# Kernel optimization log

Measured on AMD Instinct MI355X. Metric: run time of the kernel, lower is better.

Reference implementation:

```python
import jax, jax.numpy as jnp
import numpy as np

# Search geometry (matches init_kwargs)
WS, WT, PS, K, STRIDE0 = 9, 1, 7, 10, 4
SEARCH_INPUT = "noisy"
ALPHA = 0.5
CRIT = "l2"


def _extract_patches(vid, ti, hi, wi):
    """vid: [T,H,W,C]; ti/hi/wi int32 with shape [...] (patch top-left corners).
    Returns [..., PS*PS*C] with clamped (edge-replicated) boundary handling."""
    T, H, W, C = vid.shape
    dy = jnp.arange(PS)
    dx = jnp.arange(PS)
    hh = jnp.clip(hi[..., None, None] + dy[:, None], 0, H - 1)  # [...,PS,1]
    ww = jnp.clip(wi[..., None, None] + dx[None, :], 0, W - 1)  # [...,1,PS]
    p = vid[ti[..., None, None], hh, ww]  # [...,PS,PS,C]
    return p.reshape(p.shape[:-3] + (PS * PS * C,))


def _nls(vid, fflow, bflow):
    """NonLocalSearch: vid [T,H,W,C], flows [T,H,W,2] (channel 0 = x/w, 1 = y/h).
    Returns (topk_dists [nq,K], inds = (ti,hi,wi,tk,hk,wk))."""
    T, H, W, C = vid.shape
    nH, nW = H // STRIDE0, W // STRIDE0
    ti, hi, wi = jnp.meshgrid(jnp.arange(T), jnp.arange(nH) * STRIDE0,
                              jnp.arange(nW) * STRIDE0, indexing="ij")
    ti, hi, wi = ti.reshape(-1), hi.reshape(-1), wi.reshape(-1)  # [nq]
    q = _extract_patches(vid, ti, hi, wi)  # [nq, PS*PS*C]

    ff = fflow[ti, hi, wi]  # [nq,2] flow to frame t+1
    bf = bflow[ti, hi, wi]  # [nq,2] flow to frame t-1
    zero = jnp.zeros_like(ff)
    flow_dt = jnp.stack([bf, zero, ff], axis=1)  # [nq, 2*WT+1, 2] for dt=-1,0,+1
    dts = jnp.arange(-WT, WT + 1)
    tj = jnp.clip(ti[:, None] + dts[None, :], 0, T - 1)  # [nq, 2*WT+1]
    bh = jnp.clip(hi[:, None] + jnp.round(flow_dt[..., 1]).astype(jnp.int32), 0, H - 1)
    bw = jnp.clip(wi[:, None] + jnp.round(flow_dt[..., 0]).astype(jnp.int32), 0, W - 1)

    # Candidate schedule: (dt_index, oy, ox) for all (2*WT+1)*WS*WS candidates.
    r = WS // 2
    oy, ox = np.meshgrid(np.arange(-r, r + 1), np.arange(-r, r + 1), indexing="ij")
    nt = 2 * WT + 1
    specs = np.stack([np.repeat(np.arange(nt), WS * WS),
                      np.tile(oy.ravel(), nt),
                      np.tile(ox.ravel(), nt)], axis=1).astype(np.int32)  # [S,3]

    def step(_, spec):
        di, sy, sx = spec[0], spec[1], spec[2]
        tjc = tj[:, di]
        hj = jnp.clip(bh[:, di] + sy, 0, H - 1)
        wj = jnp.clip(bw[:, di] + sx, 0, W - 1)
        cp = _extract_patches(vid, tjc, hj, wj)  # [nq,D]
        d = jnp.sum((q - cp) ** 2, axis=-1)  # L2 patch distance, [nq]
        return None, (d, tjc, hj, wj)

    _, (dists, tjs, hjs, wjs) = jax.lax.scan(step, None, jnp.asarray(specs))
    # dists: [S, nq] -> top-K smallest per query
    negd, idx = jax.lax.top_k(-dists.T, K)  # [nq,K]
    tk = jnp.take_along_axis(tjs.T, idx, axis=1)
    hk = jnp.take_along_axis(hjs.T, idx, axis=1)
    wk = jnp.take_along_axis(wjs.T, idx, axis=1)
    return -negd, (ti, hi, wi, tk, hk, wk)


def _refine(vid, inds):
    """RefineSearch with wr=1,kr=1: recompute L2 patch distances at given inds."""
    ti, hi, wi, tk, hk, wk = inds
    q = _extract_patches(vid, ti, hi, wi)          # [nq, D]
    cp = _extract_patches(vid, tk, hk, wk)         # [nq, K, D]
    return jnp.sum((q[:, None, :] - cp) ** 2, axis=-1)  # [nq, K]


def setup_inputs() -> dict:
    key = jax.random.key(0)
    k1, k2, k3, k4 = jax.random.split(key, 4)
    B, T, C, H, W = 1, 5, 3, 384, 384
    noisy = jax.random.normal(k1, (B, T, C, H, W), dtype=jnp.float32)
    deno = jax.random.normal(k2, (B, T, C, H, W), dtype=jnp.float32)
    fflow = jax.random.normal(k3, (B, T, 2, H, W), dtype=jnp.float32)
    bflow = jax.random.normal(k4, (B, T, 2, H, W), dtype=jnp.float32)
    return {"noisy": noisy, "deno": deno, "fflow": fflow, "bflow": bflow}


def reference(noisy, deno, fflow, bflow):
    def per_video(nv, dv, ff, bf):
        nv_t = jnp.transpose(nv, (0, 2, 3, 1))  # [T,H,W,C]
        dv_t = jnp.transpose(dv, (0, 2, 3, 1))
        ff_t = jnp.transpose(ff, (0, 2, 3, 1))  # [T,H,W,2]
        bf_t = jnp.transpose(bf, (0, 2, 3, 1))
        if SEARCH_INPUT == "noisy":
            srch = nv_t
        elif SEARCH_INPUT == "deno":
            srch = dv_t
        else:  # interp
            srch = ALPHA * nv_t + (1.0 - ALPHA) * dv_t
        _, inds = _nls(srch, ff_t, bf_t)
        return _refine(nv_t, inds)  # [nq, K]

    dists = jax.vmap(per_video)(noisy, deno, fflow, bflow)  # [B, nq, K]
    if CRIT == "l1":
        return jnp.mean(jnp.sqrt(dists))
    return jnp.mean(dists)
```

## Files before the change

### kernel.cpp

```cpp
#include <hip/hip_runtime.h>

#define TT 5
#define HH 384
#define WW 384
#define CC 3
#define PS_ 7
#define WSR 4
#define NH_ 96
#define NW_ 96
#define NQ_ (TT*NH_*NW_)
#define NCAND 243
#define KK 10

#define RST 17
#define RCH (15*RST)
#define RDI (3*RCH)
#define RSZ (3*RDI)

typedef _Float16 h2v __attribute__((ext_vector_type(2)));
typedef __fp16   f2v __attribute__((ext_vector_type(2)));
union U32H2 { unsigned u; h2v h; f2v f; };

static __device__ __forceinline__ unsigned pack_f16(float a, float b) {
    U32H2 u;
#if defined(__has_builtin) && __has_builtin(__builtin_amdgcn_cvt_pkrtz)
    u.f = __builtin_amdgcn_cvt_pkrtz(a, b);
#else
    u.h.x = (_Float16)a; u.h.y = (_Float16)b;
#endif
    return u.u;
}

__global__ __launch_bounds__(256) void nls_kernel(
    const float* __restrict__ vid,
    const float* __restrict__ fflow,
    const float* __restrict__ bflow,
    float* __restrict__ ws)
{
    const int q   = blockIdx.x;
    const int tid = threadIdx.x;
    const int t   = q / (NH_*NW_);
    const int rem = q % (NH_*NW_);
    const int hi  = (rem / NW_) * 4;
    const int wi  = (rem % NW_) * 4;

    __shared__ unsigned reg_lds[RSZ];
    __shared__ unsigned qp_lds[84];
    __shared__ float    rowsum_lds[3*15*12];
    __shared__ float    dist[256];
    __shared__ float    qn_lds;

    const float ffx = fflow[((t*2+0)*HH + hi)*WW + wi];
    const float ffy = fflow[((t*2+1)*HH + hi)*WW + wi];
    const float bfx = bflow[((t*2+0)*HH + hi)*WW + wi];
    const float bfy = bflow[((t*2+1)*HH + hi)*WW + wi];

    const int tj0 = max(t-1, 0);
    const int tj2 = min(t+1, TT-1);
    const int bh0 = min(max(hi + (int)rintf(bfy), 0), HH-1);
    const int bw0 = min(max(wi + (int)rintf(bfx), 0), WW-1);
    const int bh2 = min(max(hi + (int)rintf(ffy), 0), HH-1);
    const int bw2 = min(max(wi + (int)rintf(ffx), 0), WW-1);
    const int rm0 = max(bh0-WSR,0), rm1 = max(hi-WSR,0), rm2 = max(bh2-WSR,0);
    const int cm0 = max(bw0-WSR,0), cm1 = max(wi-WSR,0), cm2 = max(bw2-WSR,0);
    const int ca0 = cm0 & ~1,       ca1 = cm1 & ~1,      ca2 = cm2 & ~1;

    for (int i = tid; i < 1215; i += 256) {
        int row = i / 9, j = i - row*9;
        int di  = row / 45; int r45 = row - di*45;
        int c   = r45 / 15; int r   = r45 - c*15;
        int tjd = (di==0)?tj0:((di==1)?t  :tj2);
        int rm  = (di==0)?rm0:((di==1)?rm1:rm2);
        int ca  = (di==0)?ca0:((di==1)?ca1:ca2);
        int rr  = min(rm + r, HH-1);
        const float* vrow = vid + (size_t)((tjd*CC+c)*HH + rr)*WW;
        float v0, v1;
        if (ca < 367) {
            float2 p = *(const float2*)(vrow + ca + 2*j);
            v0 = p.x; v1 = p.y;
        } else {
            v0 = vrow[min(ca+2*j,   WW-1)];
            v1 = vrow[min(ca+2*j+1, WW-1)];
        }
        reg_lds[row*RST + j] = pack_f16(v0, v1);
    }
    if (tid < 84) {
        int c  = tid / 28;
        int rr = tid - c*28;
        int dy = rr >> 2;
        int k  = rr & 3;
        int row = min(hi+dy, HH-1);
        const float* vrow = vid + (size_t)((t*CC + c)*HH + row)*WW;
        float v0 = vrow[min(wi + 2*k, WW-1)];
        float v1 = (k==3) ? 0.0f : vrow[min(wi + 2*k + 1, WW-1)];
        qp_lds[tid] = pack_f16(v0, v1);
    }
    __syncthreads();

    if (tid < 192) {
        for (int i = tid; i < 1080; i += 192) {
            int row = i >> 3, jj = i & 7;
            int base = row*RST;
            unsigned a0 = reg_lds[base + jj];
            unsigned a1 = reg_lds[base + jj + 1];
            reg_lds[base + 9 + jj] = (a0 >> 16) | (a1 << 16);
        }
    } else if (tid < 237) {
        int rid = tid - 192;
        int di = rid / 15, r = rid - di*15;
        float s[16];
        #pragma unroll
        for (int x = 0; x < 16; x++) s[x] = 0.f;
        #pragma unroll
        for (int c = 0; c < 3; c++) {
            int base = (di*3+c)*RCH + r*RST;
            #pragma unroll
            for (int j = 0; j < 8; j++) {
                U32H2 u; u.u = reg_lds[base + j];
                float lo = (float)u.h.x, hh = (float)u.h.y;
                s[2*j]   = fmaf(lo, lo, s[2*j]);
                s[2*j+1] = fmaf(hh, hh, s[2*j+1]);
            }
        }
        float rs = s[0]+s[1]+s[2]+s[3]+s[4]+s[5]+s[6];
        int ob = (di*15 + r)*12;
        rowsum_lds[ob] = rs;
        #pragma unroll
        for (int x0 = 1; x0 < 10; x0++) {
            rs += s[x0+6] - s[x0-1];
            rowsum_lds[ob + x0] = rs;
        }
    } else if (tid == 248) {
        float qn = 0.f;
        #pragma unroll
        for (int k = 0; k < 84; k++) {
            U32H2 u; u.u = qp_lds[k];
            qn = __builtin_amdgcn_fdot2(u.h, u.h, qn, false);
        }
        qn_lds = qn;
    }
    __syncthreads();

    float dmy = __int_as_float(0x7f800000);
    if (tid < NCAND) {
        int di  = tid / 81; int s81 = tid - di*81;
        int syq = s81 / 9;  int sx  = s81 - syq*9 - WSR;
        int sy  = syq - WSR;
        int bhd = (di==0)?bh0:((di==1)?hi :bh2);
        int bwd = (di==0)?bw0:((di==1)?wi :bw2);
        int rm  = (di==0)?rm0:((di==1)?rm1:rm2);
        int ca  = (di==0)?ca0:((di==1)?ca1:ca2);
        int hj = min(max(bhd + sy, 0), HH-1);
        int wj = min(max(bwd + sx, 0), WW-1);
        int roff = hj - rm;
        int wof  = wj - ca;
        int cb   = (wof >> 1) + (wof & 1)*9;
        float dot = 0.f;
        #pragma unroll
        for (int c = 0; c < 3; c++) {
            const unsigned* rc = reg_lds + (di*3+c)*RCH + roff*RST + cb;
            const unsigned* qc = qp_lds + c*28;
            #pragma unroll
            for (int dy = 0; dy < 7; dy++) {
                #pragma unroll
                for (int k = 0; k < 4; k++) {
                    U32H2 a, b;
                    a.u = rc[dy*RST + k];
                    b.u = qc[dy*4 + k];
                    dot = __builtin_amdgcn_fdot2(a.h, b.h, dot, false);
                }
            }
        }
        float c2 = 0.f;
        int rb = (di*15 + roff)*12 + wof;
        #pragma unroll
        for (int i = 0; i < 7; i++) c2 += rowsum_lds[rb + i*12];
        dmy = fmaxf(fmaf(-2.f, dot, qn_lds + c2), 0.f);
    }
    dist[tid] = dmy;
    __syncthreads();

    if (tid < 64) {
        float v0 = dist[tid], v1 = dist[tid+64], v2 = dist[tid+128], v3 = dist[tid+192];
        unsigned k0 = (__float_as_uint(v0) & 0xFFFFFF00u) | (unsigned)tid;
        unsigned k1 = (__float_as_uint(v1) & 0xFFFFFF00u) | (unsigned)(tid+64);
        unsigned k2 = (__float_as_uint(v2) & 0xFFFFFF00u) | (unsigned)(tid+128);
        unsigned k3 = (__float_as_uint(v3) & 0xFFFFFF00u) | (unsigned)(tid+192);
        float sumk = 0.f;
        #pragma unroll 1
        for (int k = 0; k < KK; k++) {
            unsigned m = min(min(k0,k1), min(k2,k3));
            #pragma unroll
            for (int ofs = 1; ofs < 64; ofs <<= 1)
                m = min(m, (unsigned)__shfl_xor((int)m, ofs, 64));
            int slot = (int)(m & 0xFFu);
            int lw = slot & 63, jw = slot >> 6;
            float vj = (jw==0)?v0:((jw==1)?v1:((jw==2)?v2:v3));
            sumk += __shfl(vj, lw, 64);
            bool me = (tid == lw);
            if (me && jw==0) k0 = 0xFFFFFFFFu;
            if (me && jw==1) k1 = 0xFFFFFFFFu;
            if (me && jw==2) k2 = 0xFFFFFFFFu;
            if (me && jw==3) k3 = 0xFFFFFFFFu;
        }
        if (tid == 0) ws[q] = sumk;
    }
}

__global__ __launch_bounds__(1024) void reduce_kernel(
    const float* __restrict__ ws, float* __restrict__ out)
{
    __shared__ float sdata[1024];
    float s = 0.0f;
    for (int i = threadIdx.x; i < NQ_; i += 1024) s += ws[i];
    sdata[threadIdx.x] = s;
    __syncthreads();
    for (int ofs = 512; ofs > 0; ofs >>= 1) {
        if ((int)threadIdx.x < ofs) sdata[threadIdx.x] += sdata[threadIdx.x + ofs];
        __syncthreads();
    }
    if (threadIdx.x == 0) out[0] = sdata[0] * (1.0f / (float)(NQ_ * KK));
}

extern "C" void kernel_launch(void* const* d_in, const int* in_sizes, int n_in,
                              void* d_out, int out_size, void* d_ws, size_t ws_size,
                              hipStream_t stream) {
    const float* noisy = (const float*)d_in[0];
    const float* fflow = (const float*)d_in[2];
    const float* bflow = (const float*)d_in[3];
    float* ws  = (float*)d_ws;
    float* out = (float*)d_out;

    nls_kernel<<<NQ_, 256, 0, stream>>>(noisy, fflow, bflow, ws);
    reduce_kernel<<<1, 1024, 0, stream>>>(ws, out);
}
```

Baseline: 314.9 us.

## Compute per-row squared-difference partials directly and reduce in parallel with atomics

Replaces the expansion ||q||^2 + ||c||^2 - 2 q·c with direct squared-difference row sums. Each of 189 threads computes, for one (frame, row offset, patch row), the 10 horizontal-shift partial SSDs using packed fp16 subtraction and fdot2. Each candidate then only sums 7 precomputed values from LDS. The odd-shift duplicate region in LDS is dropped, global loads widen to 8 floats per thread with uint4 LDS stores, and the single-block final reduction becomes a multi-block shuffle reduction with atomicAdd after a memset. The change moves the per-candidate dot-product work into shared row partials. In exchange it adds an extra memset launch and fp16 subtraction, which changes rounding, and atomic accumulation makes the final sum order nondeterministic.

Measured after the change: 283.9 us. 9.8% less time.

```diff
diff --git a/kernel.cpp b/kernel.cpp
--- a/kernel.cpp
+++ b/kernel.cpp
@@ -4,7 +4,6 @@
 #define HH 384
 #define WW 384
 #define CC 3
-#define PS_ 7
 #define WSR 4
 #define NH_ 96
 #define NW_ 96
@@ -12,10 +11,8 @@
 #define NCAND 243
 #define KK 10
 
-#define RST 17
-#define RCH (15*RST)
-#define RDI (3*RCH)
-#define RSZ (3*RDI)
+#define RROW 12
+#define RSST 13
 
 typedef _Float16 h2v __attribute__((ext_vector_type(2)));
 typedef __fp16   f2v __attribute__((ext_vector_type(2)));
@@ -44,11 +41,10 @@
     const int hi  = (rem / NW_) * 4;
     const int wi  = (rem % NW_) * 4;
 
-    __shared__ unsigned reg_lds[RSZ];
-    __shared__ unsigned qp_lds[84];
-    __shared__ float    rowsum_lds[3*15*12];
-    __shared__ float    dist[256];
-    __shared__ float    qn_lds;
+    __shared__ alignas(16) unsigned reg_lds[135*RROW];
+    __shared__ alignas(16) unsigned qp_lds[84];
+    __shared__ alignas(16) float    rssd[189*RSST];
+    __shared__ float dist[256];
 
     const float ffx = fflow[((t*2+0)*HH + hi)*WW + wi];
     const float ffy = fflow[((t*2+1)*HH + hi)*WW + wi];
@@ -65,8 +61,8 @@
     const int cm0 = max(bw0-WSR,0), cm1 = max(wi-WSR,0), cm2 = max(bw2-WSR,0);
     const int ca0 = cm0 & ~1,       ca1 = cm1 & ~1,      ca2 = cm2 & ~1;
 
-    for (int i = tid; i < 1215; i += 256) {
-        int row = i / 9, j = i - row*9;
+    for (int i = tid; i < 270; i += 256) {
+        int row = i >> 1, h = i & 1;
         int di  = row / 45; int r45 = row - di*45;
         int c   = r45 / 15; int r   = r45 - c*15;
         int tjd = (di==0)?tj0:((di==1)?t  :tj2);
@@ -74,15 +70,24 @@
         int ca  = (di==0)?ca0:((di==1)?ca1:ca2);
         int rr  = min(rm + r, HH-1);
         const float* vrow = vid + (size_t)((tjd*CC+c)*HH + rr)*WW;
-        float v0, v1;
-        if (ca < 367) {
-            float2 p = *(const float2*)(vrow + ca + 2*j);
-            v0 = p.x; v1 = p.y;
+        int c0 = ca + 8*h;
+        float f0,f1,f2,f3,f4,f5,f6,f7;
+        if (ca <= 368) {
+            float2 p0 = *(const float2*)(vrow + c0);
+            float2 p1 = *(const float2*)(vrow + c0 + 2);
+            float2 p2 = *(const float2*)(vrow + c0 + 4);
+            float2 p3 = *(const float2*)(vrow + c0 + 6);
+            f0=p0.x; f1=p0.y; f2=p1.x; f3=p1.y; f4=p2.x; f5=p2.y; f6=p3.x; f7=p3.y;
         } else {
-            v0 = vrow[min(ca+2*j,   WW-1)];
-            v1 = vrow[min(ca+2*j+1, WW-1)];
+            f0=vrow[min(c0,  WW-1)]; f1=vrow[min(c0+1,WW-1)];
+            f2=vrow[min(c0+2,WW-1)]; f3=vrow[min(c0+3,WW-1)];
+            f4=vrow[min(c0+4,WW-1)]; f5=vrow[min(c0+5,WW-1)];
+            f6=vrow[min(c0+6,WW-1)]; f7=vrow[min(c0+7,WW-1)];
         }
-        reg_lds[row*RST + j] = pack_f16(v0, v1);
+        uint4 w;
+        w.x = pack_f16(f0,f1); w.y = pack_f16(f2,f3);
+        w.z = pack_f16(f4,f5); w.w = pack_f16(f6,f7);
+        *(uint4*)&reg_lds[row*RROW + 4*h] = w;
     }
     if (tid < 84) {
         int c  = tid / 28;
@@ -97,47 +102,50 @@
     }
     __syncthreads();
 
-    if (tid < 192) {
-        for (int i = tid; i < 1080; i += 192) {
-            int row = i >> 3, jj = i & 7;
-            int base = row*RST;
-            unsigned a0 = reg_lds[base + jj];
-            unsigned a1 = reg_lds[base + jj + 1];
-            reg_lds[base + 9 + jj] = (a0 >> 16) | (a1 << 16);
-        }
-    } else if (tid < 237) {
-        int rid = tid - 192;
-        int di = rid / 15, r = rid - di*15;
-        float s[16];
-        #pragma unroll
-        for (int x = 0; x < 16; x++) s[x] = 0.f;
+    if (tid < 189) {
+        int di   = tid / 63; int r63 = tid - di*63;
+        int roff = r63 / 7;  int dy  = r63 - roff*7;
+        int rr   = roff + dy;
+        float rs[10];
+        #pragma unroll
+        for (int w = 0; w < 10; w++) rs[w] = 0.f;
         #pragma unroll
         for (int c = 0; c < 3; c++) {
-            int base = (di*3+c)*RCH + r*RST;
+            int base = ((di*3 + c)*15 + rr)*RROW;
+            uint4 va0 = *(const uint4*)&reg_lds[base];
+            uint4 va1 = *(const uint4*)&reg_lds[base + 4];
+            uint4 vq  = *(const uint4*)&qp_lds[c*28 + dy*4];
+            unsigned A[8], B[8];
+            A[0]=va0.x; A[1]=va0.y; A[2]=va0.z; A[3]=va0.w;
+            A[4]=va1.x; A[5]=va1.y; A[6]=va1.z; A[7]=va1.w;
             #pragma unroll
-            for (int j = 0; j < 8; j++) {
-                U32H2 u; u.u = reg_lds[base + j];
-                float lo = (float)u.h.x, hh = (float)u.h.y;
-                s[2*j]   = fmaf(lo, lo, s[2*j]);
-                s[2*j+1] = fmaf(hh, hh, s[2*j+1]);
+            for (int j = 0; j < 7; j++) B[j] = (A[j] >> 16) | (A[j+1] << 16);
+            B[7] = A[7] >> 16;
+            U32H2 q0,q1,q2,q3;
+            q0.u = vq.x; q1.u = vq.y; q2.u = vq.z; q3.u = vq.w;
+            #pragma unroll
+            for (int w = 0; w < 10; w++) {
+                const int off = w >> 1;
+                U32H2 c0,c1,c2,c3;
+                if (w & 1) { c0.u=B[off]; c1.u=B[off+1]; c2.u=B[off+2]; c3.u=B[off+3]; }
+                else       { c0.u=A[off]; c1.u=A[off+1]; c2.u=A[off+2]; c3.u=A[off+3]; }
+                U32H2 d0,d1,d2,d3;
+                d0.h = c0.h - q0.h;
+                d1.h = c1.h - q1.h;
+                d2.h = c2.h - q2.h;
+                d3.h = c3.h - q3.h;
+                d3.u &= 0x0000FFFFu;
+                float s = rs[w];
+                s = __builtin_amdgcn_fdot2(d0.h, d0.h, s, false);
+                s = __builtin_amdgcn_fdot2(d1.h, d1.h, s, false);
+                s = __builtin_amdgcn_fdot2(d2.h, d2.h, s, false);
+                s = __builtin_amdgcn_fdot2(d3.h, d3.h, s, false);
+                rs[w] = s;
             }
         }
-        float rs = s[0]+s[1]+s[2]+s[3]+s[4]+s[5]+s[6];
-        int ob = (di*15 + r)*12;
-        rowsum_lds[ob] = rs;
-        #pragma unroll
-        for (int x0 = 1; x0 < 10; x0++) {
-            rs += s[x0+6] - s[x0-1];
-            rowsum_lds[ob + x0] = rs;
-        }
-    } else if (tid == 248) {
-        float qn = 0.f;
-        #pragma unroll
-        for (int k = 0; k < 84; k++) {
-            U32H2 u; u.u = qp_lds[k];
-            qn = __builtin_amdgcn_fdot2(u.h, u.h, qn, false);
-        }
-        qn_lds = qn;
+        int ob = tid * RSST;
+        #pragma unroll
+        for (int w = 0; w < 10; w++) rssd[ob + w] = rs[w];
     }
     __syncthreads();
 
@@ -154,28 +162,11 @@
         int wj = min(max(bwd + sx, 0), WW-1);
         int roff = hj - rm;
         int wof  = wj - ca;
-        int cb   = (wof >> 1) + (wof & 1)*9;
-        float dot = 0.f;
-        #pragma unroll
-        for (int c = 0; c < 3; c++) {
-            const unsigned* rc = reg_lds + (di*3+c)*RCH + roff*RST + cb;
-            const unsigned* qc = qp_lds + c*28;
-            #pragma unroll
-            for (int dy = 0; dy < 7; dy++) {
-                #pragma unroll
-                for (int k = 0; k < 4; k++) {
-                    U32H2 a, b;
-                    a.u = rc[dy*RST + k];
-                    b.u = qc[dy*4 + k];
-                    dot = __builtin_amdgcn_fdot2(a.h, b.h, dot, false);
-                }
-            }
-        }
-        float c2 = 0.f;
-        int rb = (di*15 + roff)*12 + wof;
-        #pragma unroll
-        for (int i = 0; i < 7; i++) c2 += rowsum_lds[rb + i*12];
-        dmy = fmaxf(fmaf(-2.f, dot, qn_lds + c2), 0.f);
+        int ib = (di*63 + roff*7)*RSST + wof;
+        float s = 0.f;
+        #pragma unroll
+        for (int dy = 0; dy < 7; dy++) s += rssd[ib + dy*RSST];
+        dmy = s;
     }
     dist[tid] = dmy;
     __syncthreads();
@@ -207,19 +198,20 @@
     }
 }
 
-__global__ __launch_bounds__(1024) void reduce_kernel(
+__global__ __launch_bounds__(256) void reduce1_kernel(
     const float* __restrict__ ws, float* __restrict__ out)
 {
-    __shared__ float sdata[1024];
-    float s = 0.0f;
-    for (int i = threadIdx.x; i < NQ_; i += 1024) s += ws[i];
-    sdata[threadIdx.x] = s;
-    __syncthreads();
-    for (int ofs = 512; ofs > 0; ofs >>= 1) {
-        if ((int)threadIdx.x < ofs) sdata[threadIdx.x] += sdata[threadIdx.x + ofs];
-        __syncthreads();
-    }
-    if (threadIdx.x == 0) out[0] = sdata[0] * (1.0f / (float)(NQ_ * KK));
+    float s = ws[blockIdx.x*256 + threadIdx.x];
+    #pragma unroll
+    for (int o = 32; o > 0; o >>= 1) s += __shfl_down(s, o, 64);
+    __shared__ float sd[4];
+    int w = threadIdx.x >> 6, l = threadIdx.x & 63;
+    if (l == 0) sd[w] = s;
+    __syncthreads();
+    if (threadIdx.x == 0) {
+        float tot = sd[0] + sd[1] + sd[2] + sd[3];
+        atomicAdd(out, tot * (1.0f / ((float)NQ_ * (float)KK)));
+    }
 }
 
 extern "C" void kernel_launch(void* const* d_in, const int* in_sizes, int n_in,
@@ -231,6 +223,7 @@
     float* ws  = (float*)d_ws;
     float* out = (float*)d_out;
 
+    hipMemsetAsync(out, 0, sizeof(float), stream);
     nls_kernel<<<NQ_, 256, 0, stream>>>(noisy, fflow, bflow, ws);
-    reduce_kernel<<<1, 1024, 0, stream>>>(ws, out);
-}
+    reduce1_kernel<<<NQ_/256, 256, 0, stream>>>(ws, out);
+}
```
